# Optimization experiments

Measured on AMD Instinct MI355X. Metric: run time of the kernel, lower is better.

## Reference

```python
import jax, jax.numpy as jnp
import numpy as np

B, S, E, HD = 32, 1024, 768, 64
NUM_IMAGE_PATCHES = 49


def setup_inputs() -> dict:
    key = jax.random.key(0)
    ks = jax.random.split(key, 9)
    w = 0.02
    return {
        "decoder_sequence": jax.random.normal(ks[0], (B, S, E), dtype=jnp.float32),
        "Wq": jax.random.normal(ks[1], (E, HD), dtype=jnp.float32) * w,
        "bq": jnp.zeros((HD,), dtype=jnp.float32),
        "Wk": jax.random.normal(ks[2], (E, HD), dtype=jnp.float32) * w,
        "bk": jnp.zeros((HD,), dtype=jnp.float32),
        "Wv": jax.random.normal(ks[3], (E, HD), dtype=jnp.float32) * w,
        "bv": jnp.zeros((HD,), dtype=jnp.float32),
        "input_sequence_length": 975,
        "padding_mask": jax.random.randint(ks[4], (B, 1, S), 0, 2).astype(bool),
    }


def reference(decoder_sequence, Wq, bq, Wk, bk, Wv, bv, input_sequence_length, padding_mask):
    # single-head projections: [B,S,E] @ [E,HD] -> [B,S,HD]
    Q = decoder_sequence @ Wq + bq
    K = decoder_sequence @ Wk + bk
    V = decoder_sequence @ Wv + bv

    scores = jnp.einsum('bid,bjd->bij', Q, K) / jnp.sqrt(jnp.float32(HD))

    # mask: image-patch rows (i < 49) fully unmasked; text region is causal
    # (mask[49:,49:] = triu(-inf, diag=1)), i.e. -inf where i >= 49 and j > i.
    i = jnp.arange(S)[:, None]
    j = jnp.arange(S)[None, :]
    causal_bad = (i >= NUM_IMAGE_PATCHES) & (j > i)  # [S,S]
    scores = jnp.where(causal_bad[None, :, :], -jnp.inf, scores)

    # padding mask on keys, broadcast over queries: [B,1,S] -> [B,S,S]
    scores = jnp.where(padding_mask, -jnp.inf, scores)

    A = jax.nn.softmax(scores, axis=-1)
    H = jnp.einsum('bij,bjd->bid', A, V)
    return H
```

## Files before the change

kernel.cpp:

```cpp
#include <hip/hip_runtime.h>
#include <stdint.h>
#include <stddef.h>


typedef __attribute__((ext_vector_type(8))) short bf16x8;
typedef __attribute__((ext_vector_type(4))) float f32x4;

#define NIP 49
#define QSCALE 0.18033688011112042f

#define GLDS16(g, l)                                      \
  __builtin_amdgcn_global_load_lds(                       \
      (const __attribute__((address_space(1))) void*)(g), \
      (__attribute__((address_space(3))) void*)(l), 16, 0, 0)

__device__ __forceinline__ short f2b(float f) {
  union { float f; uint32_t u; } c; c.f = f;
  uint32_t u = c.u;
  uint32_t r = (u + 0x7fffu + ((u >> 16) & 1u)) >> 16;
  return (short)(uint16_t)r;
}

__global__ __launch_bounds__(256) void wt_kernel(
    const float* __restrict__ Wq, const float* __restrict__ Wk,
    const float* __restrict__ Wv, short* __restrict__ Wt) {
  int idx = blockIdx.x * 256 + threadIdx.x;
  int n = idx / 768;
  int k = idx - n * 768;
  const float* W = (n < 64) ? Wq : (n < 128) ? Wk : Wv;
  Wt[idx] = f2b(W[(size_t)k * 64 + (n & 63)]);
}

__global__ __launch_bounds__(256, 2) void proj_kernel(
    const float* __restrict__ X, const float* __restrict__ bq,
    const float* __restrict__ bk, const float* __restrict__ bv,
    const short* __restrict__ Wt, short* __restrict__ Qg,
    short* __restrict__ Kg, short* __restrict__ Vt) {
  __shared__ short lX[2][2][64][32];
  __shared__ short lW[2][2][192][32];
  const int tid = threadIdx.x;
  const int wid = tid >> 6, lane = tid & 63;
  const int l15 = lane & 15, q4 = lane >> 4;
  const int r0 = blockIdx.x * 64;

  float4 rx[4];
  auto xload = [&](int kb) {
#pragma unroll
    for (int i = 0; i < 4; ++i) {
      const int xi = tid + i * 256;
      rx[i] = *(const float4*)(X + (size_t)(r0 + (xi >> 4)) * 768 + kb + (xi & 15) * 4);
    }
  };
  auto xstage = [&](int buf) {
#pragma unroll
    for (int i = 0; i < 4; ++i) {
      const int xi = tid + i * 256;
      short4 s;
      s.x = f2b(rx[i].x); s.y = f2b(rx[i].y); s.z = f2b(rx[i].z); s.w = f2b(rx[i].w);
      *(short4*)&lX[buf][(xi & 15) >> 3][xi >> 4][(xi & 7) * 4] = s;
    }
  };
  const int wr = lane >> 2, wc = (lane & 3) * 8;
  auto wlds = [&](int buf, int kb) {
#pragma unroll
    for (int i = 0; i < 6; ++i) {
      const int fi = wid * 6 + i;
      const int j = fi >> 1, ks = fi & 1;
      GLDS16(Wt + (size_t)(j * 16 + wr) * 768 + kb + ks * 32 + wc,
             &lW[buf][ks][j * 16][0]);
    }
  };

  f32x4 acc[12];
#pragma unroll
  for (int c = 0; c < 12; ++c) acc[c] = (f32x4){0.f, 0.f, 0.f, 0.f};

  xload(0);
  wlds(0, 0);
  xstage(0);
  __syncthreads();

#pragma unroll
  for (int st = 0; st < 12; ++st) {
    const int cur = st & 1;
    if (st + 1 < 12) {
      xload((st + 1) * 64);
      wlds(cur ^ 1, (st + 1) * 64);
    }
#pragma unroll
    for (int ks = 0; ks < 2; ++ks) {
      bf16x8 a = *(const bf16x8*)&lX[cur][ks][wid * 16 + l15][q4 * 8];
#pragma unroll
      for (int c = 0; c < 12; ++c) {
        bf16x8 bw = *(const bf16x8*)&lW[cur][ks][c * 16 + l15][q4 * 8];
        acc[c] = __builtin_amdgcn_mfma_f32_16x16x32_bf16(a, bw, acc[c], 0, 0, 0);
      }
    }
    if (st + 1 < 12) xstage(cur ^ 1);
    __syncthreads();
  }

  const int b = r0 >> 10, s0 = r0 & 1023;
#pragma unroll
  for (int c = 0; c < 12; ++c) {
    const int mtx = c >> 2;
    const int h = (c & 3) * 16 + l15;
    if (mtx < 2) {
      const float bias = (mtx == 0 ? bq : bk)[h];
      short* op = (mtx == 0) ? Qg : Kg;
#pragma unroll
      for (int rr = 0; rr < 4; ++rr) {
        int row = r0 + wid * 16 + q4 * 4 + rr;
        float v = acc[c][rr] + bias;
        if (mtx == 0) v *= QSCALE;
        op[(size_t)row * 64 + h] = f2b(v);
      }
    } else {
      const float bias = bv[h];
      short4 sv;
      sv.x = f2b(acc[c][0] + bias); sv.y = f2b(acc[c][1] + bias);
      sv.z = f2b(acc[c][2] + bias); sv.w = f2b(acc[c][3] + bias);
      *(short4*)(Vt + ((size_t)(b * 64 + h) << 10) + s0 + wid * 16 + q4 * 4) = sv;
    }
  }
}

__global__ __launch_bounds__(256, 2) void attn_kernel(
    const short* __restrict__ Qg, const short* __restrict__ Kg,
    const short* __restrict__ Vt, const int* __restrict__ pad,
    float* __restrict__ out) {
  __shared__ short lK[2][2][128][32];
  __shared__ short lV[2][4][64][32];
  __shared__ short lP[4][16][68];
  __shared__ short lOnes[16][32];

  const int b = blockIdx.x;
  const int level = blockIdx.y;
  const int t = (level == 0) ? 0 : 16 - level;
  const int tid = threadIdx.x;
  const int wid = tid >> 6, lane = tid & 63;
  const int l15 = lane & 15, q4 = lane >> 4;
  const int qs = t * 64;
  const size_t base = (size_t)b * 1024;
  const int nkt = (t == 0) ? 8 : (t / 2 + 1);

  {
    int i0 = tid, i1 = tid + 256;
    ((short*)lOnes)[i0] = ((i0 >> 5) == 0) ? (short)0x3F80 : (short)0;
    if (i1 < 512) ((short*)lOnes)[i1] = ((i1 >> 5) == 0) ? (short)0x3F80 : (short)0;
  }

  const short* qrow = Qg + (base + qs + wid * 16 + l15) * 64;
  bf16x8 aq0 = *(const bf16x8*)(qrow + q4 * 8);
  bf16x8 aq1 = *(const bf16x8*)(qrow + 32 + q4 * 8);

  const int sr = lane >> 2, sc = (lane & 3) * 8;
  auto wlds_tile = [&](int buf, int kt) {
    const int kb = kt * 128;
#pragma unroll
    for (int i = 0; i < 4; ++i) {
      const int dh = i & 1, krow = wid * 32 + (i >> 1) * 16;
      GLDS16(Kg + (base + kb + krow + sr) * 64 + dh * 32 + sc,
             &lK[buf][dh][krow][0]);
    }
#pragma unroll
    for (int kq = 0; kq < 4; ++kq) {
      GLDS16(Vt + ((size_t)(b * 64 + wid * 16 + sr) << 10) + kb + kq * 32 + sc,
             &lV[buf][kq][wid * 16][0]);
    }
  };
  int pc[8];
  auto pload = [&](int kt) {
#pragma unroll
    for (int c = 0; c < 8; ++c) pc[c] = pad[base + kt * 128 + c * 16 + l15];
  };

  pload(0);
  wlds_tile(0, 0);
  __syncthreads();

  f32x4 o[5];
#pragma unroll
  for (int c = 0; c < 5; ++c) o[c] = (f32x4){0.f, 0.f, 0.f, 0.f};

  for (int kt = 0; kt < nkt; ++kt) {
    const int cur = kt & 1;
    const int kb = kt * 128;
    float padm[8];
#pragma unroll
    for (int c = 0; c < 8; ++c) padm[c] = (pc[c] != 0) ? 0.f : 1.f;
    if (kt + 1 < nkt) {
      wlds_tile(cur ^ 1, kt + 1);
      pload(kt + 1);
    }

    f32x4 s4[8];
#pragma unroll
    for (int c = 0; c < 8; ++c) {
      s4[c] = (f32x4){0.f, 0.f, 0.f, 0.f};
      bf16x8 b0 = *(const bf16x8*)&lK[cur][0][c * 16 + l15][q4 * 8];
      s4[c] = __builtin_amdgcn_mfma_f32_16x16x32_bf16(aq0, b0, s4[c], 0, 0, 0);
      bf16x8 b1 = *(const bf16x8*)&lK[cur][1][c * 16 + l15][q4 * 8];
      s4[c] = __builtin_amdgcn_mfma_f32_16x16x32_bf16(aq1, b1, s4[c], 0, 0, 0);
    }

    const bool diag = (t == 0) ? (kt == 0) : (kt == nkt - 1);
    const bool img = (t == 0 && kt > 0);
    float p[8][4];
#pragma unroll
    for (int rr = 0; rr < 4; ++rr) {
      const int qi = qs + wid * 16 + q4 * 4 + rr;
#pragma unroll
      for (int c = 0; c < 8; ++c) {
        float pv = exp2f(fminf(s4[c][rr], 80.f)) * padm[c];
        if (diag) {
          int j = kb + c * 16 + l15;
          if (qi >= NIP && j > qi) pv = 0.f;
        }
        if (img && qi >= NIP) pv = 0.f;
        p[c][rr] = pv;
      }
    }

#pragma unroll
    for (int half = 0; half < 2; ++half) {
#pragma unroll
      for (int rr = 0; rr < 4; ++rr)
#pragma unroll
        for (int c = 0; c < 4; ++c)
          lP[wid][q4 * 4 + rr][c * 16 + l15] = f2b(p[half * 4 + c][rr]);
      bf16x8 ap0 = *(const bf16x8*)&lP[wid][l15][q4 * 8];
      bf16x8 ap1 = *(const bf16x8*)&lP[wid][l15][32 + q4 * 8];
      const int kq0 = half * 2, kq1 = half * 2 + 1;
#pragma unroll
      for (int c = 0; c < 5; ++c) {
        bf16x8 b0 = (c < 4) ? *(const bf16x8*)&lV[cur][kq0][c * 16 + l15][q4 * 8]
                            : *(const bf16x8*)&lOnes[l15][q4 * 8];
        o[c] = __builtin_amdgcn_mfma_f32_16x16x32_bf16(ap0, b0, o[c], 0, 0, 0);
        bf16x8 b1 = (c < 4) ? *(const bf16x8*)&lV[cur][kq1][c * 16 + l15][q4 * 8]
                            : *(const bf16x8*)&lOnes[l15][q4 * 8];
        o[c] = __builtin_amdgcn_mfma_f32_16x16x32_bf16(ap1, b1, o[c], 0, 0, 0);
      }
    }
    __syncthreads();
  }

#pragma unroll
  for (int rr = 0; rr < 4; ++rr) {
    float l = __shfl(o[4][rr], lane & 48, 64);
    const float inv = (l > 0.f) ? 1.0f / l : 0.f;
    const size_t row = base + qs + wid * 16 + q4 * 4 + rr;
#pragma unroll
    for (int c = 0; c < 4; ++c)
      out[row * 64 + c * 16 + l15] = o[c][rr] * inv;
  }
}

extern "C" void kernel_launch(void* const* d_in, const int* in_sizes, int n_in,
                              void* d_out, int out_size, void* d_ws, size_t ws_size,
                              hipStream_t stream) {
  const float* X  = (const float*)d_in[0];
  const float* Wq = (const float*)d_in[1];
  const float* bq = (const float*)d_in[2];
  const float* Wk = (const float*)d_in[3];
  const float* bk = (const float*)d_in[4];
  const float* Wv = (const float*)d_in[5];
  const float* bv = (const float*)d_in[6];
  const int* pad  = (const int*)d_in[8];
  float* out = (float*)d_out;

  short* Qg = (short*)d_ws;
  short* Kg = Qg + 32768 * 64;
  short* Vt = Kg + 32768 * 64;
  short* Wt = Vt + 32768 * 64;

  wt_kernel<<<576, 256, 0, stream>>>(Wq, Wk, Wv, Wt);
  proj_kernel<<<512, 256, 0, stream>>>(X, bq, bk, bv, Wt, Qg, Kg, Vt);
  attn_kernel<<<dim3(32, 16), 256, 0, stream>>>(Qg, Kg, Vt, pad, out);
}
```

Before: 200.9 us.

## Compute transposed scores to keep P in registers via permlane swaps

Swaps the MFMA operands so the score tile comes out transposed, with each lane holding consecutive key positions. P can then be packed to bf16 with v_cvt_pk_bf16_f32 and rearranged into the A operand with permlane32/16 swaps, removing the LDS round trip through lP. The padding mask is precomputed as an additive -16384 float bias and used as the accumulator's initial value, which replaces the per-element multiply. Projection-side bf16 conversions also use the packed hardware convert. The risk is correctness of the lane permutation and reliance on gfx950-specific instructions.

```diff
diff --git a/kernel.cpp b/kernel.cpp
--- a/kernel.cpp
+++ b/kernel.cpp
@@ -21,14 +21,22 @@
   return (short)(uint16_t)r;
 }
 
+__device__ __forceinline__ uint32_t pk2(float lo, float hi) {
+  uint32_t r;
+  asm("v_cvt_pk_bf16_f32 %0, %1, %2" : "=v"(r) : "v"(lo), "v"(hi));
+  return r;
+}
+
 __global__ __launch_bounds__(256) void wt_kernel(
     const float* __restrict__ Wq, const float* __restrict__ Wk,
-    const float* __restrict__ Wv, short* __restrict__ Wt) {
+    const float* __restrict__ Wv, const int* __restrict__ pad,
+    short* __restrict__ Wt, float* __restrict__ padneg) {
   int idx = blockIdx.x * 256 + threadIdx.x;
   int n = idx / 768;
   int k = idx - n * 768;
   const float* W = (n < 64) ? Wq : (n < 128) ? Wk : Wv;
   Wt[idx] = f2b(W[(size_t)k * 64 + (n & 63)]);
+  if (idx < 32768) padneg[idx] = pad[idx] ? -16384.f : 0.f;
 }
 
 __global__ __launch_bounds__(256, 2) void proj_kernel(
@@ -55,9 +63,10 @@
 #pragma unroll
     for (int i = 0; i < 4; ++i) {
       const int xi = tid + i * 256;
-      short4 s;
-      s.x = f2b(rx[i].x); s.y = f2b(rx[i].y); s.z = f2b(rx[i].z); s.w = f2b(rx[i].w);
-      *(short4*)&lX[buf][(xi & 15) >> 3][xi >> 4][(xi & 7) * 4] = s;
+      uint2 s;
+      s.x = pk2(rx[i].x, rx[i].y);
+      s.y = pk2(rx[i].z, rx[i].w);
+      *(uint2*)&lX[buf][(xi & 15) >> 3][xi >> 4][(xi & 7) * 4] = s;
     }
   };
   const int wr = lane >> 2, wc = (lane & 3) * 8;
@@ -117,21 +126,20 @@
       }
     } else {
       const float bias = bv[h];
-      short4 sv;
-      sv.x = f2b(acc[c][0] + bias); sv.y = f2b(acc[c][1] + bias);
-      sv.z = f2b(acc[c][2] + bias); sv.w = f2b(acc[c][3] + bias);
-      *(short4*)(Vt + ((size_t)(b * 64 + h) << 10) + s0 + wid * 16 + q4 * 4) = sv;
+      uint2 sv;
+      sv.x = pk2(acc[c][0] + bias, acc[c][1] + bias);
+      sv.y = pk2(acc[c][2] + bias, acc[c][3] + bias);
+      *(uint2*)(Vt + ((size_t)(b * 64 + h) << 10) + s0 + wid * 16 + q4 * 4) = sv;
     }
   }
 }
 
 __global__ __launch_bounds__(256, 2) void attn_kernel(
     const short* __restrict__ Qg, const short* __restrict__ Kg,
-    const short* __restrict__ Vt, const int* __restrict__ pad,
+    const short* __restrict__ Vt, const float* __restrict__ padneg,
     float* __restrict__ out) {
   __shared__ short lK[2][2][128][32];
   __shared__ short lV[2][4][64][32];
-  __shared__ short lP[4][16][68];
   __shared__ short lOnes[16][32];
 
   const int b = blockIdx.x;
@@ -151,8 +159,9 @@
   }
 
   const short* qrow = Qg + (base + qs + wid * 16 + l15) * 64;
-  bf16x8 aq0 = *(const bf16x8*)(qrow + q4 * 8);
-  bf16x8 aq1 = *(const bf16x8*)(qrow + 32 + q4 * 8);
+  bf16x8 bq0 = *(const bf16x8*)(qrow + q4 * 8);
+  bf16x8 bq1 = *(const bf16x8*)(qrow + 32 + q4 * 8);
+  const int qi = qs + wid * 16 + l15;
 
   const int sr = lane >> 2, sc = (lane & 3) * 8;
   auto wlds_tile = [&](int buf, int kt) {
@@ -169,13 +178,15 @@
              &lV[buf][kq][wid * 16][0]);
     }
   };
-  int pc[8];
-  auto pload = [&](int kt) {
-#pragma unroll
-    for (int c = 0; c < 8; ++c) pc[c] = pad[base + kt * 128 + c * 16 + l15];
-  };
-
-  pload(0);
+
+  float4 pnv[8];
+  auto pnload = [&](int kt) {
+#pragma unroll
+    for (int c = 0; c < 8; ++c)
+      pnv[c] = *(const float4*)(padneg + base + kt * 128 + c * 16 + q4 * 4);
+  };
+
+  pnload(0);
   wlds_tile(0, 0);
   __syncthreads();
 
@@ -186,60 +197,60 @@
   for (int kt = 0; kt < nkt; ++kt) {
     const int cur = kt & 1;
     const int kb = kt * 128;
-    float padm[8];
-#pragma unroll
-    for (int c = 0; c < 8; ++c) padm[c] = (pc[c] != 0) ? 0.f : 1.f;
+
+    f32x4 s4[8];
+#pragma unroll
+    for (int c = 0; c < 8; ++c)
+      s4[c] = (f32x4){pnv[c].x, pnv[c].y, pnv[c].z, pnv[c].w};
+
     if (kt + 1 < nkt) {
       wlds_tile(cur ^ 1, kt + 1);
-      pload(kt + 1);
-    }
-
-    f32x4 s4[8];
+      pnload(kt + 1);
+    }
+
 #pragma unroll
     for (int c = 0; c < 8; ++c) {
-      s4[c] = (f32x4){0.f, 0.f, 0.f, 0.f};
-      bf16x8 b0 = *(const bf16x8*)&lK[cur][0][c * 16 + l15][q4 * 8];
-      s4[c] = __builtin_amdgcn_mfma_f32_16x16x32_bf16(aq0, b0, s4[c], 0, 0, 0);
-      bf16x8 b1 = *(const bf16x8*)&lK[cur][1][c * 16 + l15][q4 * 8];
-      s4[c] = __builtin_amdgcn_mfma_f32_16x16x32_bf16(aq1, b1, s4[c], 0, 0, 0);
+      bf16x8 a0 = *(const bf16x8*)&lK[cur][0][c * 16 + l15][q4 * 8];
+      s4[c] = __builtin_amdgcn_mfma_f32_16x16x32_bf16(a0, bq0, s4[c], 0, 0, 0);
+      bf16x8 a1 = *(const bf16x8*)&lK[cur][1][c * 16 + l15][q4 * 8];
+      s4[c] = __builtin_amdgcn_mfma_f32_16x16x32_bf16(a1, bq1, s4[c], 0, 0, 0);
     }
 
     const bool diag = (t == 0) ? (kt == 0) : (kt == nkt - 1);
     const bool img = (t == 0 && kt > 0);
-    float p[8][4];
-#pragma unroll
-    for (int rr = 0; rr < 4; ++rr) {
-      const int qi = qs + wid * 16 + q4 * 4 + rr;
-#pragma unroll
-      for (int c = 0; c < 8; ++c) {
-        float pv = exp2f(fminf(s4[c][rr], 80.f)) * padm[c];
+#pragma unroll
+    for (int c = 0; c < 8; ++c) {
+#pragma unroll
+      for (int rr = 0; rr < 4; ++rr) {
+        float pv = exp2f(fminf(s4[c][rr], 80.f));
         if (diag) {
-          int j = kb + c * 16 + l15;
+          int j = kb + c * 16 + q4 * 4 + rr;
           if (qi >= NIP && j > qi) pv = 0.f;
         }
-        if (img && qi >= NIP) pv = 0.f;
-        p[c][rr] = pv;
-      }
-    }
-
-#pragma unroll
-    for (int half = 0; half < 2; ++half) {
-#pragma unroll
-      for (int rr = 0; rr < 4; ++rr)
-#pragma unroll
-        for (int c = 0; c < 4; ++c)
-          lP[wid][q4 * 4 + rr][c * 16 + l15] = f2b(p[half * 4 + c][rr]);
-      bf16x8 ap0 = *(const bf16x8*)&lP[wid][l15][q4 * 8];
-      bf16x8 ap1 = *(const bf16x8*)&lP[wid][l15][32 + q4 * 8];
-      const int kq0 = half * 2, kq1 = half * 2 + 1;
+        if (img) {
+          if (qi >= NIP) pv = 0.f;
+        }
+        s4[c][rr] = pv;
+      }
+    }
+
+#pragma unroll
+    for (int m = 0; m < 4; ++m) {
+      uint32_t w0 = pk2(s4[2 * m][0], s4[2 * m][1]);
+      uint32_t w1 = pk2(s4[2 * m][2], s4[2 * m][3]);
+      uint32_t w2 = pk2(s4[2 * m + 1][0], s4[2 * m + 1][1]);
+      uint32_t w3 = pk2(s4[2 * m + 1][2], s4[2 * m + 1][3]);
+      asm("v_permlane32_swap_b32 %0, %1" : "+v"(w0), "+v"(w2));
+      asm("v_permlane32_swap_b32 %0, %1" : "+v"(w1), "+v"(w3));
+      asm("v_permlane16_swap_b32 %0, %1" : "+v"(w0), "+v"(w2));
+      asm("v_permlane16_swap_b32 %0, %1" : "+v"(w1), "+v"(w3));
+      union { uint32_t u[4]; bf16x8 v; } af;
+      af.u[0] = w0; af.u[1] = w1; af.u[2] = w2; af.u[3] = w3;
 #pragma unroll
       for (int c = 0; c < 5; ++c) {
-        bf16x8 b0 = (c < 4) ? *(const bf16x8*)&lV[cur][kq0][c * 16 + l15][q4 * 8]
+        bf16x8 bv = (c < 4) ? *(const bf16x8*)&lV[cur][m][c * 16 + l15][q4 * 8]
                             : *(const bf16x8*)&lOnes[l15][q4 * 8];
-        o[c] = __builtin_amdgcn_mfma_f32_16x16x32_bf16(ap0, b0, o[c], 0, 0, 0);
-        bf16x8 b1 = (c < 4) ? *(const bf16x8*)&lV[cur][kq1][c * 16 + l15][q4 * 8]
-                            : *(const bf16x8*)&lOnes[l15][q4 * 8];
-        o[c] = __builtin_amdgcn_mfma_f32_16x16x32_bf16(ap1, b1, o[c], 0, 0, 0);
+        o[c] = __builtin_amdgcn_mfma_f32_16x16x32_bf16(af.v, bv, o[c], 0, 0, 0);
       }
     }
     __syncthreads();
@@ -273,8 +284,9 @@
   short* Kg = Qg + 32768 * 64;
   short* Vt = Kg + 32768 * 64;
   short* Wt = Vt + 32768 * 64;
-
-  wt_kernel<<<576, 256, 0, stream>>>(Wq, Wk, Wv, Wt);
+  float* padneg = (float*)(Wt + 147456);
+
+  wt_kernel<<<576, 256, 0, stream>>>(Wq, Wk, Wv, pad, Wt, padneg);
   proj_kernel<<<512, 256, 0, stream>>>(X, bq, bk, bv, Wt, Qg, Kg, Vt);
-  attn_kernel<<<dim3(32, 16), 256, 0, stream>>>(Qg, Kg, Vt, pad, out);
-}
+  attn_kernel<<<dim3(32, 16), 256, 0, stream>>>(Qg, Kg, Vt, padneg, out);
+}
```

Result: no change. 199.6 us (-0.6%).
